# Performance work log

Hardware: AMD Instinct MI355X
Metric: run time of the kernel (lower is better)

## Reference

```python
import jax, jax.numpy as jnp
import numpy as np

N_SEGMENTS = 1024
D_IN = 16
WIDTH = 128
LATENT = 128
DOT = 64
HEADS = 4
N = 500000


def setup_inputs() -> dict:
    key = jax.random.key(0)
    ks = jax.random.split(key, 12)
    he = lambda k, shape: jax.random.normal(k, shape, jnp.float32) * np.sqrt(2.0 / shape[0])
    inputs = jax.random.normal(ks[0], (N, D_IN), jnp.float32)
    segment_ids = jnp.sort(jax.random.randint(ks[1], (N,), 0, N_SEGMENTS))
    lengths = jax.random.randint(ks[2], (N_SEGMENTS,), 0, 1000)
    return {
        "inputs": inputs,
        "segment_ids": segment_ids,
        "lengths": lengths,
        "W0": he(ks[3], (D_IN, WIDTH)), "b0": jnp.zeros((WIDTH,), jnp.float32),
        "W1": he(ks[4], (WIDTH, WIDTH)), "b1": jnp.zeros((WIDTH,), jnp.float32),
        "Wlat": he(ks[5], (WIDTH, LATENT)), "blat": jnp.zeros((LATENT,), jnp.float32),
        "Wrho": he(ks[6], (LATENT, LATENT)), "brho": jnp.zeros((LATENT,), jnp.float32),
        "W_k": he(ks[7], (LATENT + D_IN, DOT * HEADS)),
        # W_q is zero-initialized in the original; use small random for a non-degenerate test
        "W_q": jax.random.normal(ks[8], (HEADS, DOT), jnp.float32) * 0.02,
    }


def reference(inputs, segment_ids, lengths, W0, b0, W1, b1, Wlat, blat, Wrho, brho, W_k, W_q):
    # psi: Dense(width,relu) x n_layers, then Dense(latent,relu)
    h = jax.nn.relu(inputs @ W0 + b0)            # [N, width]
    h = jax.nn.relu(h @ W1 + b1)                 # [N, width]
    enc = jax.nn.relu(h @ Wlat + blat)           # [N, latent]
    # segment mean aggregation
    ones = jnp.ones((enc.shape[0],), enc.dtype)
    counts = jax.ops.segment_sum(ones, segment_ids, num_segments=N_SEGMENTS)
    seg_sum = jax.ops.segment_sum(enc, segment_ids, num_segments=N_SEGMENTS)
    agg = seg_sum / jnp.maximum(counts, 1.0)[:, None]   # [S, latent]
    # rho
    agg = jax.nn.relu(agg @ Wrho + brho)         # [S, latent]
    # scatter back and concat with raw inputs
    combined = jnp.concatenate([inputs, agg[segment_ids]], axis=-1)  # [N, d+latent]
    # keys: [N, heads, dot] (tf.split over last dim == reshape to (heads, dot))
    keys = (combined @ W_k).reshape(-1, HEADS, DOT)
    pre = jnp.einsum('nhd,hd->nh', keys, W_q) / np.sqrt(float(DOT))  # [N, heads]
    # per-head segment softmax (inference: no attention dropout)
    seg_max = jax.ops.segment_max(pre, segment_ids, num_segments=N_SEGMENTS)
    e = jnp.exp(pre - seg_max[segment_ids])
    denom = jax.ops.segment_sum(e, segment_ids, num_segments=N_SEGMENTS)
    attn = e / denom[segment_ids]                # [N, heads]
    return attn
```

## Files before the change

### kernel.cpp

```cpp
#include <hip/hip_runtime.h>

#define NN 500000
#define NSEG 1024
#define MAXE 2048

__launch_bounds__(256, 4)
__global__ void attn_kernel(const float* __restrict__ x,
                            const int* __restrict__ seg,
                            const float* __restrict__ Wk,
                            const float* __restrict__ Wq,
                            float* __restrict__ out) {
  __shared__ float4 sPre[MAXE];
  __shared__ float sVx[64];
  __shared__ float red[4][4];
  __shared__ float bc[4];
  __shared__ int rng[2];

  int s = blockIdx.x, t = threadIdx.x;

  if (t < 64) {
    int c = t >> 2, h = t & 3;
    float a = 0.f;
#pragma unroll 8
    for (int d = 0; d < 64; ++d)
      a = fmaf(Wk[c * 256 + h * 64 + d], Wq[h * 64 + d], a);
    sVx[t] = a * 0.125f;
  }
  if (t < 2) {
    int target = s + t;
    int lo_ = 0, hi_ = NN;
    while (lo_ < hi_) {
      int mid = (lo_ + hi_) >> 1;
      if (seg[mid] < target) lo_ = mid + 1; else hi_ = mid;
    }
    rng[t] = lo_;
  }
  __syncthreads();

  int lo = rng[0], hi = rng[1], len = hi - lo;
  if (len <= 0) return;
  int w = t >> 6;
  const float4* sVx4 = (const float4*)sVx;

  if (len <= MAXE) {
    float m0 = -1e30f, m1 = -1e30f, m2 = -1e30f, m3 = -1e30f;
    for (int i = t; i < len; i += 256) {
      const float4* xp = (const float4*)(x + (size_t)(lo + i) * 16);
      float4 a0 = xp[0], a1 = xp[1], a2 = xp[2], a3 = xp[3];
      float xv[16] = {a0.x,a0.y,a0.z,a0.w, a1.x,a1.y,a1.z,a1.w,
                      a2.x,a2.y,a2.z,a2.w, a3.x,a3.y,a3.z,a3.w};
      float p0 = 0.f, p1 = 0.f, p2 = 0.f, p3 = 0.f;
#pragma unroll
      for (int k = 0; k < 16; ++k) {
        float4 vh = sVx4[k];
        p0 = fmaf(xv[k], vh.x, p0);
        p1 = fmaf(xv[k], vh.y, p1);
        p2 = fmaf(xv[k], vh.z, p2);
        p3 = fmaf(xv[k], vh.w, p3);
      }
      sPre[i] = (float4){p0, p1, p2, p3};
      m0 = fmaxf(m0, p0); m1 = fmaxf(m1, p1);
      m2 = fmaxf(m2, p2); m3 = fmaxf(m3, p3);
    }
    for (int o = 1; o < 64; o <<= 1) {
      m0 = fmaxf(m0, __shfl_xor(m0, o)); m1 = fmaxf(m1, __shfl_xor(m1, o));
      m2 = fmaxf(m2, __shfl_xor(m2, o)); m3 = fmaxf(m3, __shfl_xor(m3, o));
    }
    if ((t & 63) == 0) { red[w][0]=m0; red[w][1]=m1; red[w][2]=m2; red[w][3]=m3; }
    __syncthreads();
    if (t < 4) bc[t] = fmaxf(fmaxf(red[0][t], red[1][t]), fmaxf(red[2][t], red[3][t]));
    __syncthreads();
    float M0 = bc[0], M1 = bc[1], M2 = bc[2], M3 = bc[3];

    float s0 = 0.f, s1 = 0.f, s2 = 0.f, s3 = 0.f;
    for (int i = t; i < len; i += 256) {
      float4 p = sPre[i];
      float4 e = { __expf(p.x - M0), __expf(p.y - M1),
                   __expf(p.z - M2), __expf(p.w - M3) };
      sPre[i] = e;
      s0 += e.x; s1 += e.y; s2 += e.z; s3 += e.w;
    }
    for (int o = 1; o < 64; o <<= 1) {
      s0 += __shfl_xor(s0, o); s1 += __shfl_xor(s1, o);
      s2 += __shfl_xor(s2, o); s3 += __shfl_xor(s3, o);
    }
    __syncthreads();
    if ((t & 63) == 0) { red[w][0]=s0; red[w][1]=s1; red[w][2]=s2; red[w][3]=s3; }
    __syncthreads();
    if (t < 4) bc[t] = 1.f / (red[0][t] + red[1][t] + red[2][t] + red[3][t]);
    __syncthreads();
    float i0 = bc[0], i1 = bc[1], i2 = bc[2], i3 = bc[3];

    for (int i = t; i < len; i += 256) {
      float4 e = sPre[i];
      e.x *= i0; e.y *= i1; e.z *= i2; e.w *= i3;
      *(float4*)(out + (size_t)(lo + i) * 4) = e;
    }
  } else {
    float m0 = -1e30f, m1 = -1e30f, m2 = -1e30f, m3 = -1e30f;
    for (int i = t; i < len; i += 256) {
      const float4* xp = (const float4*)(x + (size_t)(lo + i) * 16);
      float4 a0 = xp[0], a1 = xp[1], a2 = xp[2], a3 = xp[3];
      float xv[16] = {a0.x,a0.y,a0.z,a0.w, a1.x,a1.y,a1.z,a1.w,
                      a2.x,a2.y,a2.z,a2.w, a3.x,a3.y,a3.z,a3.w};
      float p0 = 0.f, p1 = 0.f, p2 = 0.f, p3 = 0.f;
#pragma unroll
      for (int k = 0; k < 16; ++k) {
        float4 vh = sVx4[k];
        p0 = fmaf(xv[k], vh.x, p0);
        p1 = fmaf(xv[k], vh.y, p1);
        p2 = fmaf(xv[k], vh.z, p2);
        p3 = fmaf(xv[k], vh.w, p3);
      }
      *(float4*)(out + (size_t)(lo + i) * 4) = (float4){p0, p1, p2, p3};
      m0 = fmaxf(m0, p0); m1 = fmaxf(m1, p1);
      m2 = fmaxf(m2, p2); m3 = fmaxf(m3, p3);
    }
    for (int o = 1; o < 64; o <<= 1) {
      m0 = fmaxf(m0, __shfl_xor(m0, o)); m1 = fmaxf(m1, __shfl_xor(m1, o));
      m2 = fmaxf(m2, __shfl_xor(m2, o)); m3 = fmaxf(m3, __shfl_xor(m3, o));
    }
    if ((t & 63) == 0) { red[w][0]=m0; red[w][1]=m1; red[w][2]=m2; red[w][3]=m3; }
    __syncthreads();
    if (t < 4) bc[t] = fmaxf(fmaxf(red[0][t], red[1][t]), fmaxf(red[2][t], red[3][t]));
    __syncthreads();
    float M0 = bc[0], M1 = bc[1], M2 = bc[2], M3 = bc[3];

    float s0 = 0.f, s1 = 0.f, s2 = 0.f, s3 = 0.f;
    for (int i = t; i < len; i += 256) {
      float4 p = *(const float4*)(out + (size_t)(lo + i) * 4);
      float4 e = { __expf(p.x - M0), __expf(p.y - M1),
                   __expf(p.z - M2), __expf(p.w - M3) };
      *(float4*)(out + (size_t)(lo + i) * 4) = e;
      s0 += e.x; s1 += e.y; s2 += e.z; s3 += e.w;
    }
    for (int o = 1; o < 64; o <<= 1) {
      s0 += __shfl_xor(s0, o); s1 += __shfl_xor(s1, o);
      s2 += __shfl_xor(s2, o); s3 += __shfl_xor(s3, o);
    }
    __syncthreads();
    if ((t & 63) == 0) { red[w][0]=s0; red[w][1]=s1; red[w][2]=s2; red[w][3]=s3; }
    __syncthreads();
    if (t < 4) bc[t] = 1.f / (red[0][t] + red[1][t] + red[2][t] + red[3][t]);
    __syncthreads();
    float i0 = bc[0], i1 = bc[1], i2 = bc[2], i3 = bc[3];

    for (int i = t; i < len; i += 256) {
      float4 e = *(const float4*)(out + (size_t)(lo + i) * 4);
      e.x *= i0; e.y *= i1; e.z *= i2; e.w *= i3;
      *(float4*)(out + (size_t)(lo + i) * 4) = e;
    }
  }
}

extern "C" void kernel_launch(void* const* d_in, const int* in_sizes, int n_in,
                              void* d_out, int out_size, void* d_ws, size_t ws_size,
                              hipStream_t stream) {
  const float* x   = (const float*)d_in[0];
  const int*   seg = (const int*)  d_in[1];
  const float* Wk  = (const float*)d_in[11];
  const float* Wq  = (const float*)d_in[12];
  float* out = (float*)d_out;

  hipLaunchKernelGGL(attn_kernel, dim3(NSEG), dim3(256), 0, stream,
                     x, seg, Wk, Wq, out);
}
```

Measured before the change: 106.9 us.

## Drop softmax max pass, use wave-parallel segment search, keep values in registers

```diff
diff --git a/kernel.cpp b/kernel.cpp
--- a/kernel.cpp
+++ b/kernel.cpp
@@ -2,7 +2,7 @@
 
 #define NN 500000
 #define NSEG 1024
-#define MAXE 2048
+#define REGC 4
 
 __launch_bounds__(256, 4)
 __global__ void attn_kernel(const float* __restrict__ x,
@@ -10,40 +10,94 @@
                             const float* __restrict__ Wk,
                             const float* __restrict__ Wq,
                             float* __restrict__ out) {
-  __shared__ float4 sPre[MAXE];
   __shared__ float sVx[64];
+  __shared__ int   rng[2];
   __shared__ float red[4][4];
-  __shared__ float bc[4];
-  __shared__ int rng[2];
+  __shared__ float bc4[4];
 
   int s = blockIdx.x, t = threadIdx.x;
+  int wv = t >> 6, lane = t & 63;
 
-  if (t < 64) {
-    int c = t >> 2, h = t & 3;
+  if (wv < 2) {
+    int target = s + wv;
+    int lo = 0, hi = NN, r = -1;
+    while (true) {
+      int width = hi - lo;
+      if (width <= 0) { r = lo; break; }
+      if (width <= 64) {
+        int pos = lo + lane;
+        bool lt = (pos < hi) && (seg[pos] < target);
+        r = lo + __popcll(__ballot(lt));
+        break;
+      }
+      int step = (width + 63) >> 6;
+      int pos = lo + lane * step;
+      bool lt = (pos < hi) && (seg[pos] < target);
+      int c = __popcll(__ballot(lt));
+      if (c == 0) { r = lo; break; }
+      hi = min(lo + c * step, hi);
+      lo = lo + (c - 1) * step + 1;
+    }
+    if (lane == 0) rng[wv] = r;
+  } else if (wv == 2) {
+    int c = lane >> 2, h = lane & 3;
     float a = 0.f;
 #pragma unroll 8
     for (int d = 0; d < 64; ++d)
       a = fmaf(Wk[c * 256 + h * 64 + d], Wq[h * 64 + d], a);
-    sVx[t] = a * 0.125f;
-  }
-  if (t < 2) {
-    int target = s + t;
-    int lo_ = 0, hi_ = NN;
-    while (lo_ < hi_) {
-      int mid = (lo_ + hi_) >> 1;
-      if (seg[mid] < target) lo_ = mid + 1; else hi_ = mid;
-    }
-    rng[t] = lo_;
+    sVx[lane] = a * 0.125f;
   }
   __syncthreads();
 
   int lo = rng[0], hi = rng[1], len = hi - lo;
   if (len <= 0) return;
-  int w = t >> 6;
   const float4* sVx4 = (const float4*)sVx;
 
-  if (len <= MAXE) {
-    float m0 = -1e30f, m1 = -1e30f, m2 = -1e30f, m3 = -1e30f;
+  if (len <= REGC * 256) {
+    float4 e[REGC];
+    float s0 = 0.f, s1 = 0.f, s2 = 0.f, s3 = 0.f;
+#pragma unroll
+    for (int it = 0; it < REGC; ++it) {
+      int i = t + it * 256;
+      if (i < len) {
+        const float4* xp = (const float4*)(x + (size_t)(lo + i) * 16);
+        float4 a0 = xp[0], a1 = xp[1], a2 = xp[2], a3 = xp[3];
+        float xv[16] = {a0.x,a0.y,a0.z,a0.w, a1.x,a1.y,a1.z,a1.w,
+                        a2.x,a2.y,a2.z,a2.w, a3.x,a3.y,a3.z,a3.w};
+        float p0 = 0.f, p1 = 0.f, p2 = 0.f, p3 = 0.f;
+#pragma unroll
+        for (int k = 0; k < 16; ++k) {
+          float4 vh = sVx4[k];
+          p0 = fmaf(xv[k], vh.x, p0);
+          p1 = fmaf(xv[k], vh.y, p1);
+          p2 = fmaf(xv[k], vh.z, p2);
+          p3 = fmaf(xv[k], vh.w, p3);
+        }
+        float4 ev = { __expf(p0), __expf(p1), __expf(p2), __expf(p3) };
+        e[it] = ev;
+        s0 += ev.x; s1 += ev.y; s2 += ev.z; s3 += ev.w;
+      }
+    }
+    for (int o = 1; o < 64; o <<= 1) {
+      s0 += __shfl_xor(s0, o); s1 += __shfl_xor(s1, o);
+      s2 += __shfl_xor(s2, o); s3 += __shfl_xor(s3, o);
+    }
+    if (lane == 0) { red[wv][0]=s0; red[wv][1]=s1; red[wv][2]=s2; red[wv][3]=s3; }
+    __syncthreads();
+    if (t < 4) bc4[t] = 1.f / (red[0][t] + red[1][t] + red[2][t] + red[3][t]);
+    __syncthreads();
+    float i0 = bc4[0], i1 = bc4[1], i2 = bc4[2], i3 = bc4[3];
+#pragma unroll
+    for (int it = 0; it < REGC; ++it) {
+      int i = t + it * 256;
+      if (i < len) {
+        float4 ev = e[it];
+        ev.x *= i0; ev.y *= i1; ev.z *= i2; ev.w *= i3;
+        *(float4*)(out + (size_t)(lo + i) * 4) = ev;
+      }
+    }
+  } else {
+    float s0 = 0.f, s1 = 0.f, s2 = 0.f, s3 = 0.f;
     for (int i = t; i < len; i += 256) {
       const float4* xp = (const float4*)(x + (size_t)(lo + i) * 16);
       float4 a0 = xp[0], a1 = xp[1], a2 = xp[2], a3 = xp[3];
@@ -58,97 +112,23 @@
         p2 = fmaf(xv[k], vh.z, p2);
         p3 = fmaf(xv[k], vh.w, p3);
       }
-      sPre[i] = (float4){p0, p1, p2, p3};
-      m0 = fmaxf(m0, p0); m1 = fmaxf(m1, p1);
-      m2 = fmaxf(m2, p2); m3 = fmaxf(m3, p3);
-    }
-    for (int o = 1; o < 64; o <<= 1) {
-      m0 = fmaxf(m0, __shfl_xor(m0, o)); m1 = fmaxf(m1, __shfl_xor(m1, o));
-      m2 = fmaxf(m2, __shfl_xor(m2, o)); m3 = fmaxf(m3, __shfl_xor(m3, o));
-    }
-    if ((t & 63) == 0) { red[w][0]=m0; red[w][1]=m1; red[w][2]=m2; red[w][3]=m3; }
-    __syncthreads();
-    if (t < 4) bc[t] = fmaxf(fmaxf(red[0][t], red[1][t]), fmaxf(red[2][t], red[3][t]));
-    __syncthreads();
-    float M0 = bc[0], M1 = bc[1], M2 = bc[2], M3 = bc[3];
-
-    float s0 = 0.f, s1 = 0.f, s2 = 0.f, s3 = 0.f;
-    for (int i = t; i < len; i += 256) {
-      float4 p = sPre[i];
-      float4 e = { __expf(p.x - M0), __expf(p.y - M1),
-                   __expf(p.z - M2), __expf(p.w - M3) };
-      sPre[i] = e;
-      s0 += e.x; s1 += e.y; s2 += e.z; s3 += e.w;
+      float4 ev = { __expf(p0), __expf(p1), __expf(p2), __expf(p3) };
+      *(float4*)(out + (size_t)(lo + i) * 4) = ev;
+      s0 += ev.x; s1 += ev.y; s2 += ev.z; s3 += ev.w;
     }
     for (int o = 1; o < 64; o <<= 1) {
       s0 += __shfl_xor(s0, o); s1 += __shfl_xor(s1, o);
       s2 += __shfl_xor(s2, o); s3 += __shfl_xor(s3, o);
     }
+    if (lane == 0) { red[wv][0]=s0; red[wv][1]=s1; red[wv][2]=s2; red[wv][3]=s3; }
     __syncthreads();
-    if ((t & 63) == 0) { red[w][0]=s0; red[w][1]=s1; red[w][2]=s2; red[w][3]=s3; }
+    if (t < 4) bc4[t] = 1.f / (red[0][t] + red[1][t] + red[2][t] + red[3][t]);
     __syncthreads();
-    if (t < 4) bc[t] = 1.f / (red[0][t] + red[1][t] + red[2][t] + red[3][t]);
-    __syncthreads();
-    float i0 = bc[0], i1 = bc[1], i2 = bc[2], i3 = bc[3];
-
+    float i0 = bc4[0], i1 = bc4[1], i2 = bc4[2], i3 = bc4[3];
     for (int i = t; i < len; i += 256) {
-      float4 e = sPre[i];
-      e.x *= i0; e.y *= i1; e.z *= i2; e.w *= i3;
-      *(float4*)(out + (size_t)(lo + i) * 4) = e;
-    }
-  } else {
-    float m0 = -1e30f, m1 = -1e30f, m2 = -1e30f, m3 = -1e30f;
-    for (int i = t; i < len; i += 256) {
-      const float4* xp = (const float4*)(x + (size_t)(lo + i) * 16);
-      float4 a0 = xp[0], a1 = xp[1], a2 = xp[2], a3 = xp[3];
-      float xv[16] = {a0.x,a0.y,a0.z,a0.w, a1.x,a1.y,a1.z,a1.w,
-                      a2.x,a2.y,a2.z,a2.w, a3.x,a3.y,a3.z,a3.w};
-      float p0 = 0.f, p1 = 0.f, p2 = 0.f, p3 = 0.f;
-#pragma unroll
-      for (int k = 0; k < 16; ++k) {
-        float4 vh = sVx4[k];
-        p0 = fmaf(xv[k], vh.x, p0);
-        p1 = fmaf(xv[k], vh.y, p1);
-        p2 = fmaf(xv[k], vh.z, p2);
-        p3 = fmaf(xv[k], vh.w, p3);
-      }
-      *(float4*)(out + (size_t)(lo + i) * 4) = (float4){p0, p1, p2, p3};
-      m0 = fmaxf(m0, p0); m1 = fmaxf(m1, p1);
-      m2 = fmaxf(m2, p2); m3 = fmaxf(m3, p3);
-    }
-    for (int o = 1; o < 64; o <<= 1) {
-      m0 = fmaxf(m0, __shfl_xor(m0, o)); m1 = fmaxf(m1, __shfl_xor(m1, o));
-      m2 = fmaxf(m2, __shfl_xor(m2, o)); m3 = fmaxf(m3, __shfl_xor(m3, o));
-    }
-    if ((t & 63) == 0) { red[w][0]=m0; red[w][1]=m1; red[w][2]=m2; red[w][3]=m3; }
-    __syncthreads();
-    if (t < 4) bc[t] = fmaxf(fmaxf(red[0][t], red[1][t]), fmaxf(red[2][t], red[3][t]));
-    __syncthreads();
-    float M0 = bc[0], M1 = bc[1], M2 = bc[2], M3 = bc[3];
-
-    float s0 = 0.f, s1 = 0.f, s2 = 0.f, s3 = 0.f;
-    for (int i = t; i < len; i += 256) {
-      float4 p = *(const float4*)(out + (size_t)(lo + i) * 4);
-      float4 e = { __expf(p.x - M0), __expf(p.y - M1),
-                   __expf(p.z - M2), __expf(p.w - M3) };
-      *(float4*)(out + (size_t)(lo + i) * 4) = e;
-      s0 += e.x; s1 += e.y; s2 += e.z; s3 += e.w;
-    }
-    for (int o = 1; o < 64; o <<= 1) {
-      s0 += __shfl_xor(s0, o); s1 += __shfl_xor(s1, o);
-      s2 += __shfl_xor(s2, o); s3 += __shfl_xor(s3, o);
-    }
-    __syncthreads();
-    if ((t & 63) == 0) { red[w][0]=s0; red[w][1]=s1; red[w][2]=s2; red[w][3]=s3; }
-    __syncthreads();
-    if (t < 4) bc[t] = 1.f / (red[0][t] + red[1][t] + red[2][t] + red[3][t]);
-    __syncthreads();
-    float i0 = bc[0], i1 = bc[1], i2 = bc[2], i3 = bc[3];
-
-    for (int i = t; i < len; i += 256) {
-      float4 e = *(const float4*)(out + (size_t)(lo + i) * 4);
-      e.x *= i0; e.y *= i1; e.z *= i2; e.w *= i3;
-      *(float4*)(out + (size_t)(lo + i) * 4) = e;
+      float4 ev = *(const float4*)(out + (size_t)(lo + i) * 4);
+      ev.x *= i0; ev.y *= i1; ev.z *= i2; ev.w *= i3;
+      *(float4*)(out + (size_t)(lo + i) * 4) = ev;
     }
   }
 }
```

Measured after the change: 101.2 us. -5.3%, faster.
